# Kernel optimization log

Hardware: AMD Instinct MI355X
Metric: run time of the kernel (lower is better)

The kernel has to match this reference:

```python
import jax, jax.numpy as jnp
import numpy as np

B, C, H, W = 4, 64, 64, 64
E = C // 8  # embedding_channels = inChannels // k


def _conv1x1(x, w, b):
    # x:[B,C,H,W], w:[O,C], b:[O] -> [B,O,H,W]
    return jnp.einsum('bchw,oc->bohw', x, w) + b[None, :, None, None]


def setup_inputs() -> dict:
    key = jax.random.key(0)
    ks = jax.random.split(key, 10)
    s_c = 1.0 / np.sqrt(C)
    s_e = 1.0 / np.sqrt(E)
    x = jax.random.normal(ks[0], (B, C, H, W), jnp.float32)
    Wk = jax.random.normal(ks[1], (E, C), jnp.float32) * s_c
    bk = jax.random.normal(ks[2], (E,), jnp.float32) * 0.01
    Wq = jax.random.normal(ks[3], (E, C), jnp.float32) * s_c
    bq = jax.random.normal(ks[4], (E,), jnp.float32) * 0.01
    Wv = jax.random.normal(ks[5], (E, C), jnp.float32) * s_c
    bv = jax.random.normal(ks[6], (E,), jnp.float32) * 0.01
    Wo = jax.random.normal(ks[7], (C, E), jnp.float32) * s_e
    bo = jax.random.normal(ks[8], (C,), jnp.float32) * 0.01
    gamma = jax.random.normal(ks[9], (), jnp.float32) * 0.1  # module inits to 0; randomized for nontrivial math
    return {"x": x, "Wk": Wk, "bk": bk, "Wq": Wq, "bq": bq,
            "Wv": Wv, "bv": bv, "Wo": Wo, "bo": bo, "gamma": gamma}


def reference(x, Wk, bk, Wq, bq, Wv, bv, Wo, bo, gamma):
    b, c, h, w = x.shape
    n = h * w
    f = _conv1x1(x, Wk, bk).reshape(b, E, n)  # key
    g = _conv1x1(x, Wq, bq).reshape(b, E, n)  # query
    hx = _conv1x1(x, Wv, bv).reshape(b, E, n)  # value
    # s[b,i,j] = sum_e f[b,e,i] * g[b,e,j]  (bmm(f^T, g))
    s = jnp.einsum('bei,bej->bij', f, g)
    # torch softmax over dim=1 (the f/key index i)
    beta = jax.nn.softmax(s, axis=1)
    # v[b,e,j] = sum_i hx[b,e,i] * beta[b,i,j]
    v = jnp.einsum('bei,bij->bej', hx, beta).reshape(b, E, h, w)
    o = _conv1x1(v, Wo, bo)
    y = gamma * o + x
    y = jnp.where(y >= 0, y, 0.01 * y)  # LeakyReLU(0.01)
    return (y, beta)
```

## Files before the change

### kernel.cpp

```cpp
#include <hip/hip_runtime.h>


namespace {
constexpr int Bb = 4;
constexpr int Cc = 64;
constexpr int Nn = 4096;
constexpr int Ee = 8;
constexpr int WAVES = 16;
constexpr int COLS = 64;
constexpr int ISPAN = Nn / WAVES;
}

__global__ __launch_bounds__(256) void proj_kernel(
    const float* __restrict__ x,
    const float* __restrict__ Wk, const float* __restrict__ bk,
    const float* __restrict__ Wq, const float* __restrict__ bq,
    const float* __restrict__ Wv, const float* __restrict__ bv,
    float* __restrict__ fo, float* __restrict__ go, float* __restrict__ ho)
{
    __shared__ float wk[Ee * Cc], wq[Ee * Cc], wv[Ee * Cc];
    __shared__ float sb[3 * Ee];
    const int t = threadIdx.x;
    for (int i = t; i < Ee * Cc; i += 256) { wk[i] = Wk[i]; wq[i] = Wq[i]; wv[i] = Wv[i]; }
    if (t < Ee) { sb[t] = bk[t]; sb[Ee + t] = bq[t]; sb[2 * Ee + t] = bv[t]; }
    __syncthreads();

    const int gidx = blockIdx.x * 256 + t;
    const int b = gidx >> 12;
    const int n = gidx & (Nn - 1);

    float af[Ee], ag[Ee], ah[Ee];
#pragma unroll
    for (int e = 0; e < Ee; e++) { af[e] = sb[e]; ag[e] = sb[Ee + e]; ah[e] = sb[2 * Ee + e]; }

    const float* xp = x + (size_t)b * Cc * Nn + n;
#pragma unroll 4
    for (int c = 0; c < Cc; c++) {
        const float xv = xp[(size_t)c * Nn];
#pragma unroll
        for (int e = 0; e < Ee; e++) {
            af[e] = fmaf(wk[e * Cc + c], xv, af[e]);
            ag[e] = fmaf(wq[e * Cc + c], xv, ag[e]);
            ah[e] = fmaf(wv[e * Cc + c], xv, ah[e]);
        }
    }
    float4* fp = (float4*)(fo + (size_t)gidx * Ee);
    float4* gp = (float4*)(go + (size_t)gidx * Ee);
    float4* hp = (float4*)(ho + (size_t)gidx * Ee);
    fp[0] = make_float4(af[0], af[1], af[2], af[3]);
    fp[1] = make_float4(af[4], af[5], af[6], af[7]);
    gp[0] = make_float4(ag[0], ag[1], ag[2], ag[3]);
    gp[1] = make_float4(ag[4], ag[5], ag[6], ag[7]);
    hp[0] = make_float4(ah[0], ah[1], ah[2], ah[3]);
    hp[1] = make_float4(ah[4], ah[5], ah[6], ah[7]);
}

__global__ __launch_bounds__(WAVES * 64) void attn_kernel(
    const float* __restrict__ f, const float* __restrict__ g,
    const float* __restrict__ h,
    float* __restrict__ beta, float* __restrict__ v_out)
{
    const int b = blockIdx.x >> 6;
    const int jbase = (blockIdx.x & 63) * COLS;
    const int t = threadIdx.x;
    const int lane = t & 63;
    const int w = __builtin_amdgcn_readfirstlane(t >> 6);
    const int j = jbase + lane;

    const float4* gp = (const float4*)(g + ((size_t)b * Nn + j) * Ee);
    const float4 g0 = gp[0], g1 = gp[1];
    const float gq[Ee] = {g0.x, g0.y, g0.z, g0.w, g1.x, g1.y, g1.z, g1.w};

    const float* fb = f + (size_t)b * Nn * Ee;
    const float* hb = h + (size_t)b * Nn * Ee;
    const int i0 = w * ISPAN;

    float sum = 0.f;
#pragma unroll 4
    for (int ii = 0; ii < ISPAN; ii++) {
        const float4* fr = (const float4*)(fb + (size_t)(i0 + ii) * Ee);
        const float4 a0 = fr[0], a1 = fr[1];
        float s = a0.x * gq[0];
        s = fmaf(a0.y, gq[1], s); s = fmaf(a0.z, gq[2], s); s = fmaf(a0.w, gq[3], s);
        s = fmaf(a1.x, gq[4], s); s = fmaf(a1.y, gq[5], s);
        s = fmaf(a1.z, gq[6], s); s = fmaf(a1.w, gq[7], s);
        sum += __expf(s);
    }
    __shared__ float red[WAVES][COLS];
    red[w][lane] = sum;
    __syncthreads();
    float sf = 0.f;
#pragma unroll
    for (int ww = 0; ww < WAVES; ww++) sf += red[ww][lane];
    const float inv = 1.0f / sf;

    float vacc[Ee] = {0.f, 0.f, 0.f, 0.f, 0.f, 0.f, 0.f, 0.f};
    float* bp = beta + (size_t)b * Nn * Nn + (size_t)jbase + lane;
#pragma unroll 4
    for (int ii = 0; ii < ISPAN; ii++) {
        const int i = i0 + ii;
        const float4* fr = (const float4*)(fb + (size_t)i * Ee);
        const float4 a0 = fr[0], a1 = fr[1];
        float s = a0.x * gq[0];
        s = fmaf(a0.y, gq[1], s); s = fmaf(a0.z, gq[2], s); s = fmaf(a0.w, gq[3], s);
        s = fmaf(a1.x, gq[4], s); s = fmaf(a1.y, gq[5], s);
        s = fmaf(a1.z, gq[6], s); s = fmaf(a1.w, gq[7], s);
        const float p = __expf(s) * inv;
        bp[(size_t)i * Nn] = p;
        const float4* hr = (const float4*)(hb + (size_t)i * Ee);
        const float4 h0 = hr[0], h1 = hr[1];
        vacc[0] = fmaf(h0.x, p, vacc[0]); vacc[1] = fmaf(h0.y, p, vacc[1]);
        vacc[2] = fmaf(h0.z, p, vacc[2]); vacc[3] = fmaf(h0.w, p, vacc[3]);
        vacc[4] = fmaf(h1.x, p, vacc[4]); vacc[5] = fmaf(h1.y, p, vacc[5]);
        vacc[6] = fmaf(h1.z, p, vacc[6]); vacc[7] = fmaf(h1.w, p, vacc[7]);
    }

    __shared__ float vred[WAVES][COLS][Ee];
    float4* vw = (float4*)&vred[w][lane][0];
    vw[0] = make_float4(vacc[0], vacc[1], vacc[2], vacc[3]);
    vw[1] = make_float4(vacc[4], vacc[5], vacc[6], vacc[7]);
    __syncthreads();
    if (t < COLS * Ee) {
        const int col = t >> 3;
        const int e = t & 7;
        float acc = 0.f;
#pragma unroll
        for (int ww = 0; ww < WAVES; ww++) acc += vred[ww][col][e];
        v_out[((size_t)b * Nn + jbase + col) * Ee + e] = acc;
    }
}

__global__ __launch_bounds__(256) void out_kernel(
    const float* __restrict__ v, const float* __restrict__ Wo,
    const float* __restrict__ bo, const float* __restrict__ x,
    const float* __restrict__ gamma_p, float* __restrict__ y)
{
    __shared__ float wo[Cc * Ee];
    __shared__ float sbo[Cc];
    const int t = threadIdx.x;
    for (int i = t; i < Cc * Ee; i += 256) wo[i] = Wo[i];
    if (t < Cc) sbo[t] = bo[t];
    __syncthreads();
    const float gamma = gamma_p[0];

    const int gidx = blockIdx.x * 256 + t;
    const int b = gidx >> 12;
    const int n = gidx & (Nn - 1);

    const float4* vp = (const float4*)(v + (size_t)gidx * Ee);
    const float4 v0 = vp[0], v1 = vp[1];
    const float vv[Ee] = {v0.x, v0.y, v0.z, v0.w, v1.x, v1.y, v1.z, v1.w};

    const float* xp = x + (size_t)b * Cc * Nn + n;
    float* yp = y + (size_t)b * Cc * Nn + n;
#pragma unroll 4
    for (int c = 0; c < Cc; c++) {
        float o = sbo[c];
#pragma unroll
        for (int e = 0; e < Ee; e++) o = fmaf(wo[c * Ee + e], vv[e], o);
        const float t2 = fmaf(gamma, o, xp[(size_t)c * Nn]);
        yp[(size_t)c * Nn] = (t2 >= 0.f) ? t2 : 0.01f * t2;
    }
}

extern "C" void kernel_launch(void* const* d_in, const int* in_sizes, int n_in,
                              void* d_out, int out_size, void* d_ws, size_t ws_size,
                              hipStream_t stream)
{
    const float* x     = (const float*)d_in[0];
    const float* Wk    = (const float*)d_in[1];
    const float* bk    = (const float*)d_in[2];
    const float* Wq    = (const float*)d_in[3];
    const float* bq    = (const float*)d_in[4];
    const float* Wv    = (const float*)d_in[5];
    const float* bv    = (const float*)d_in[6];
    const float* Wo    = (const float*)d_in[7];
    const float* bo    = (const float*)d_in[8];
    const float* gamma = (const float*)d_in[9];

    float* y    = (float*)d_out;
    float* beta = y + (size_t)Bb * Cc * Nn;

    float* f = (float*)d_ws;
    float* g = f + (size_t)Bb * Nn * Ee;
    float* h = g + (size_t)Bb * Nn * Ee;
    float* v = h + (size_t)Bb * Nn * Ee;

    proj_kernel<<<Bb * Nn / 256, 256, 0, stream>>>(x, Wk, bk, Wq, bq, Wv, bv, f, g, h);
    attn_kernel<<<Bb * (Nn / COLS), WAVES * 64, 0, stream>>>(f, g, h, beta, v);
    out_kernel<<<Bb * Nn / 256, 256, 0, stream>>>(v, Wo, bo, x, gamma, y);
}
```

Before: 357.3 us.

## Split attention into sum and beta kernels with i-dimension split and partial reductions

```diff
diff --git a/kernel.cpp b/kernel.cpp
--- a/kernel.cpp
+++ b/kernel.cpp
@@ -6,10 +6,22 @@
 constexpr int Cc = 64;
 constexpr int Nn = 4096;
 constexpr int Ee = 8;
-constexpr int WAVES = 16;
 constexpr int COLS = 64;
-constexpr int ISPAN = Nn / WAVES;
-}
+constexpr int SPLIT = 4;
+constexpr int CHUNK = Nn / SPLIT;
+constexpr int W2 = 8;
+constexpr int IS2 = CHUNK / W2;
+constexpr float LOG2E = 1.4426950408889634f;
+}
+
+#if defined(__has_builtin)
+#if __has_builtin(__builtin_amdgcn_exp2f)
+#define EXP2F(x) __builtin_amdgcn_exp2f(x)
+#endif
+#endif
+#ifndef EXP2F
+#define EXP2F(x) exp2f(x)
+#endif
 
 __global__ __launch_bounds__(256) void proj_kernel(
     const float* __restrict__ x,
@@ -55,13 +67,13 @@
     hp[1] = make_float4(ah[4], ah[5], ah[6], ah[7]);
 }
 
-__global__ __launch_bounds__(WAVES * 64) void attn_kernel(
+__global__ __launch_bounds__(512, 8) void sums_kernel(
     const float* __restrict__ f, const float* __restrict__ g,
-    const float* __restrict__ h,
-    float* __restrict__ beta, float* __restrict__ v_out)
-{
-    const int b = blockIdx.x >> 6;
-    const int jbase = (blockIdx.x & 63) * COLS;
+    float* __restrict__ sums_part)
+{
+    const int b = blockIdx.x >> 8;
+    const int jbase = ((blockIdx.x >> 2) & 63) * COLS;
+    const int si = blockIdx.x & 3;
     const int t = threadIdx.x;
     const int lane = t & 63;
     const int w = __builtin_amdgcn_readfirstlane(t >> 6);
@@ -69,44 +81,75 @@
 
     const float4* gp = (const float4*)(g + ((size_t)b * Nn + j) * Ee);
     const float4 g0 = gp[0], g1 = gp[1];
-    const float gq[Ee] = {g0.x, g0.y, g0.z, g0.w, g1.x, g1.y, g1.z, g1.w};
+    const float gq[Ee] = {g0.x * LOG2E, g0.y * LOG2E, g0.z * LOG2E, g0.w * LOG2E,
+                          g1.x * LOG2E, g1.y * LOG2E, g1.z * LOG2E, g1.w * LOG2E};
+
+    const float* fb = f + (size_t)b * Nn * Ee;
+    const int i0 = si * CHUNK + w * IS2;
+
+    float sum = 0.f;
+#pragma unroll 4
+    for (int ii = 0; ii < IS2; ii++) {
+        const float4* fr = (const float4*)(fb + (size_t)(i0 + ii) * Ee);
+        const float4 a0 = fr[0], a1 = fr[1];
+        float sA = a0.x * gq[0];
+        sA = fmaf(a0.y, gq[1], sA); sA = fmaf(a0.z, gq[2], sA); sA = fmaf(a0.w, gq[3], sA);
+        float sB = a1.x * gq[4];
+        sB = fmaf(a1.y, gq[5], sB); sB = fmaf(a1.z, gq[6], sB); sB = fmaf(a1.w, gq[7], sB);
+        sum += EXP2F(sA + sB);
+    }
+    __shared__ float red[W2][COLS];
+    red[w][lane] = sum;
+    __syncthreads();
+    if (t < COLS) {
+        float sf = 0.f;
+#pragma unroll
+        for (int ww = 0; ww < W2; ww++) sf += red[ww][t];
+        sums_part[(size_t)si * (Bb * Nn) + (size_t)b * Nn + jbase + t] = sf;
+    }
+}
+
+__global__ __launch_bounds__(512, 4) void beta_kernel(
+    const float* __restrict__ f, const float* __restrict__ g,
+    const float* __restrict__ h, const float* __restrict__ sums_part,
+    float* __restrict__ beta, float* __restrict__ v_part)
+{
+    const int b = blockIdx.x >> 8;
+    const int jbase = ((blockIdx.x >> 2) & 63) * COLS;
+    const int si = blockIdx.x & 3;
+    const int t = threadIdx.x;
+    const int lane = t & 63;
+    const int w = __builtin_amdgcn_readfirstlane(t >> 6);
+    const int j = jbase + lane;
+
+    const float4* gp = (const float4*)(g + ((size_t)b * Nn + j) * Ee);
+    const float4 g0 = gp[0], g1 = gp[1];
+    const float gq[Ee] = {g0.x * LOG2E, g0.y * LOG2E, g0.z * LOG2E, g0.w * LOG2E,
+                          g1.x * LOG2E, g1.y * LOG2E, g1.z * LOG2E, g1.w * LOG2E};
+
+    float sf = 0.f;
+#pragma unroll
+    for (int s2 = 0; s2 < SPLIT; s2++)
+        sf += sums_part[(size_t)s2 * (Bb * Nn) + (size_t)b * Nn + j];
+    const float inv = 1.0f / sf;
 
     const float* fb = f + (size_t)b * Nn * Ee;
     const float* hb = h + (size_t)b * Nn * Ee;
-    const int i0 = w * ISPAN;
-
-    float sum = 0.f;
-#pragma unroll 4
-    for (int ii = 0; ii < ISPAN; ii++) {
-        const float4* fr = (const float4*)(fb + (size_t)(i0 + ii) * Ee);
-        const float4 a0 = fr[0], a1 = fr[1];
-        float s = a0.x * gq[0];
-        s = fmaf(a0.y, gq[1], s); s = fmaf(a0.z, gq[2], s); s = fmaf(a0.w, gq[3], s);
-        s = fmaf(a1.x, gq[4], s); s = fmaf(a1.y, gq[5], s);
-        s = fmaf(a1.z, gq[6], s); s = fmaf(a1.w, gq[7], s);
-        sum += __expf(s);
-    }
-    __shared__ float red[WAVES][COLS];
-    red[w][lane] = sum;
-    __syncthreads();
-    float sf = 0.f;
-#pragma unroll
-    for (int ww = 0; ww < WAVES; ww++) sf += red[ww][lane];
-    const float inv = 1.0f / sf;
+    const int i0 = si * CHUNK + w * IS2;
 
     float vacc[Ee] = {0.f, 0.f, 0.f, 0.f, 0.f, 0.f, 0.f, 0.f};
     float* bp = beta + (size_t)b * Nn * Nn + (size_t)jbase + lane;
 #pragma unroll 4
-    for (int ii = 0; ii < ISPAN; ii++) {
+    for (int ii = 0; ii < IS2; ii++) {
         const int i = i0 + ii;
         const float4* fr = (const float4*)(fb + (size_t)i * Ee);
         const float4 a0 = fr[0], a1 = fr[1];
-        float s = a0.x * gq[0];
-        s = fmaf(a0.y, gq[1], s); s = fmaf(a0.z, gq[2], s); s = fmaf(a0.w, gq[3], s);
-        s = fmaf(a1.x, gq[4], s); s = fmaf(a1.y, gq[5], s);
-        s = fmaf(a1.z, gq[6], s); s = fmaf(a1.w, gq[7], s);
-        const float p = __expf(s) * inv;
-        bp[(size_t)i * Nn] = p;
+        float sA = a0.x * gq[0];
+        sA = fmaf(a0.y, gq[1], sA); sA = fmaf(a0.z, gq[2], sA); sA = fmaf(a0.w, gq[3], sA);
+        float sB = a1.x * gq[4];
+        sB = fmaf(a1.y, gq[5], sB); sB = fmaf(a1.z, gq[6], sB); sB = fmaf(a1.w, gq[7], sB);
+        const float p = EXP2F(sA + sB) * inv;
+        __builtin_nontemporal_store(p, bp + (size_t)i * Nn);
         const float4* hr = (const float4*)(hb + (size_t)i * Ee);
         const float4 h0 = hr[0], h1 = hr[1];
         vacc[0] = fmaf(h0.x, p, vacc[0]); vacc[1] = fmaf(h0.y, p, vacc[1]);
@@ -115,23 +158,24 @@
         vacc[6] = fmaf(h1.z, p, vacc[6]); vacc[7] = fmaf(h1.w, p, vacc[7]);
     }
 
-    __shared__ float vred[WAVES][COLS][Ee];
+    __shared__ float vred[W2][COLS][Ee];
     float4* vw = (float4*)&vred[w][lane][0];
     vw[0] = make_float4(vacc[0], vacc[1], vacc[2], vacc[3]);
     vw[1] = make_float4(vacc[4], vacc[5], vacc[6], vacc[7]);
     __syncthreads();
-    if (t < COLS * Ee) {
+    {
         const int col = t >> 3;
         const int e = t & 7;
         float acc = 0.f;
 #pragma unroll
-        for (int ww = 0; ww < WAVES; ww++) acc += vred[ww][col][e];
-        v_out[((size_t)b * Nn + jbase + col) * Ee + e] = acc;
+        for (int ww = 0; ww < W2; ww++) acc += vred[ww][col][e];
+        v_part[(size_t)si * (Bb * Nn * Ee) +
+               ((size_t)b * Nn + jbase + col) * Ee + e] = acc;
     }
 }
 
 __global__ __launch_bounds__(256) void out_kernel(
-    const float* __restrict__ v, const float* __restrict__ Wo,
+    const float* __restrict__ v_part, const float* __restrict__ Wo,
     const float* __restrict__ bo, const float* __restrict__ x,
     const float* __restrict__ gamma_p, float* __restrict__ y)
 {
@@ -147,9 +191,14 @@
     const int b = gidx >> 12;
     const int n = gidx & (Nn - 1);
 
-    const float4* vp = (const float4*)(v + (size_t)gidx * Ee);
-    const float4 v0 = vp[0], v1 = vp[1];
-    const float vv[Ee] = {v0.x, v0.y, v0.z, v0.w, v1.x, v1.y, v1.z, v1.w};
+    float vv[Ee] = {0.f, 0.f, 0.f, 0.f, 0.f, 0.f, 0.f, 0.f};
+#pragma unroll
+    for (int si = 0; si < SPLIT; si++) {
+        const float4* vp = (const float4*)(v_part + (size_t)si * (Bb * Nn * Ee) + (size_t)gidx * Ee);
+        const float4 v0 = vp[0], v1 = vp[1];
+        vv[0] += v0.x; vv[1] += v0.y; vv[2] += v0.z; vv[3] += v0.w;
+        vv[4] += v1.x; vv[5] += v1.y; vv[6] += v1.z; vv[7] += v1.w;
+    }
 
     const float* xp = x + (size_t)b * Cc * Nn + n;
     float* yp = y + (size_t)b * Cc * Nn + n;
@@ -184,9 +233,13 @@
     float* f = (float*)d_ws;
     float* g = f + (size_t)Bb * Nn * Ee;
     float* h = g + (size_t)Bb * Nn * Ee;
-    float* v = h + (size_t)Bb * Nn * Ee;
+    float* sums_part = h + (size_t)Bb * Nn * Ee;
+    float* v_part = sums_part + (size_t)SPLIT * Bb * Nn;
+
+    const int grid2 = Bb * (Nn / COLS) * SPLIT;
 
     proj_kernel<<<Bb * Nn / 256, 256, 0, stream>>>(x, Wk, bk, Wq, bq, Wv, bv, f, g, h);
-    attn_kernel<<<Bb * (Nn / COLS), WAVES * 64, 0, stream>>>(f, g, h, beta, v);
-    out_kernel<<<Bb * Nn / 256, 256, 0, stream>>>(v, Wo, bo, x, gamma, y);
-}
+    sums_kernel<<<grid2, W2 * 64, 0, stream>>>(f, g, sums_part);
+    beta_kernel<<<grid2, W2 * 64, 0, stream>>>(f, g, h, sums_part, beta, v_part);
+    out_kernel<<<Bb * Nn / 256, 256, 0, stream>>>(v_part, Wo, bo, x, gamma, y);
+}
```

Result: faster. 347.2 us (-2.8%).
